# Optimization experiments

Hardware: AMD Instinct MI355X
Metric: run time of the kernel (lower is better)

Reference implementation:

```python
import jax, jax.numpy as jnp
import numpy as np

N = 50000
E = 800000
IN_DIM = 128
HEADS = 4
OUT_DIM = 32
LEAKY_ALPHA = 0.4
BN_EPS = 1e-5


def setup_inputs() -> dict:
    key = jax.random.key(0)
    k_x, k_e, k_w, k_as, k_at = jax.random.split(key, 5)
    x = jax.random.normal(k_x, (N, IN_DIM), dtype=jnp.float32)
    edge_index = jax.random.randint(k_e, (2, E), 0, N, dtype=jnp.int32)
    # Linear weight stored as (in_dim, heads*out_dim) so that h = x @ W
    w_bound = 1.0 / np.sqrt(IN_DIM)
    W = jax.random.uniform(k_w, (IN_DIM, HEADS * OUT_DIM), dtype=jnp.float32,
                           minval=-w_bound, maxval=w_bound)
    # xavier_uniform with gain=1.414 on (heads, out_dim)
    xav = 1.414 * np.sqrt(6.0 / (HEADS + OUT_DIM))
    a_src = jax.random.uniform(k_as, (HEADS, OUT_DIM), dtype=jnp.float32, minval=-xav, maxval=xav)
    a_tgt = jax.random.uniform(k_at, (HEADS, OUT_DIM), dtype=jnp.float32, minval=-xav, maxval=xav)
    # BatchNorm affine params (fresh init: gamma=1, beta=0)
    gamma = jnp.ones((HEADS * OUT_DIM,), dtype=jnp.float32)
    beta = jnp.zeros((HEADS * OUT_DIM,), dtype=jnp.float32)
    return {"x": x, "W": W, "a_src": a_src, "a_tgt": a_tgt,
            "gamma": gamma, "beta": beta, "edge_index": edge_index}


def reference(x, W, a_src, a_tgt, gamma, beta, edge_index):
    src = edge_index[0]
    tgt = edge_index[1]
    n = x.shape[0]
    # Linear projection -> (N, H, D)
    h = (x @ W).reshape(n, HEADS, OUT_DIM)
    h_src = h[src]   # (E, H, D)
    h_tgt = h[tgt]   # (E, H, D)
    # Per-edge, per-head attention logits
    e_src = jnp.einsum('ehd,hd->eh', h_src, a_src)
    e_tgt = jnp.einsum('ehd,hd->eh', h_tgt, a_tgt)
    e = jax.nn.leaky_relu(e_src + e_tgt, negative_slope=LEAKY_ALPHA)
    # Global (per-head) max subtraction for numerical stability, as in original
    e = e - jnp.max(e, axis=0, keepdims=True)
    alpha = jnp.exp(e)  # (E, H)
    # Segment softmax denominator over target nodes
    alpha_sum = jax.ops.segment_sum(alpha, tgt, num_segments=n) + 1e-16  # (N, H)
    alpha = alpha / alpha_sum[tgt]
    # dropout is identity in eval mode
    # Weighted aggregation of source features into targets
    h_prime = h_src * alpha[:, :, None]  # (E, H, D)
    out = jax.ops.segment_sum(h_prime, tgt, num_segments=n)  # (N, H, D)
    out = out.reshape(n, HEADS * OUT_DIM)  # concat=True
    # BatchNorm1d in training mode: biased batch statistics
    mean = jnp.mean(out, axis=0)
    var = jnp.mean(jnp.square(out - mean), axis=0)
    out = (out - mean) * jax.lax.rsqrt(var + BN_EPS) * gamma + beta
    return out
```

## Files before the change

### kernel.cpp

```cpp
#include <hip/hip_runtime.h>
#include <math.h>

#define N_NODES 50000
#define E_EDGES 800000
#define IN_DIM 128
#define HEADS 4
#define OUT_DIM 32
#define HD 128
#define LEAKY 0.4f
#define BN_EPS 1e-5f

#define BSH 7
#define NB ((N_NODES + 127) >> BSH)
#define FB 196
#define FCH 4096
#define PCAP 2560
#define SRTCAP 3072
#define SCCH ((NB + 63) / 64)
#define K1B ((N_NODES + 63) / 64)
#define K2_BLOCKS 32

typedef __attribute__((ext_vector_type(8))) short short8;
typedef __attribute__((ext_vector_type(8))) unsigned short us8;
typedef __attribute__((ext_vector_type(4))) float f32x4;

__device__ __forceinline__ unsigned enc_max(float f) {
    unsigned u = __float_as_uint(f);
    return ((int)u >= 0) ? (u | 0x80000000u) : ~u;
}
__device__ __forceinline__ float dec_max(unsigned u) {
    return (u & 0x80000000u) ? __uint_as_float(u ^ 0x80000000u)
                             : __uint_as_float(~u);
}

__device__ __forceinline__ float leaky(float v) {
    return v > 0.f ? v : LEAKY * v;
}

__device__ __forceinline__ unsigned short f2bf(float f) {
    unsigned u = __float_as_uint(f);
    u = (u + 0x7FFFu + ((u >> 16) & 1u)) >> 16;
    return (unsigned short)u;
}
__device__ __forceinline__ float bf2f(unsigned short u) {
    return __uint_as_float(((unsigned)u) << 16);
}

struct FillSh { int est[FCH]; int hist[NB]; int rbase[NB]; };
union F1Sh { unsigned short Wl[32 * 64 * 8]; FillSh fl; };

__global__ __launch_bounds__(256) void f1_gemm_fill(
    const float* __restrict__ x, const float* __restrict__ W,
    const float* __restrict__ a_src, const float* __restrict__ a_tgt,
    const int* __restrict__ src, const int* __restrict__ tgt,
    int* __restrict__ bcur, int* __restrict__ ebkt,
    unsigned short* __restrict__ hb, float* __restrict__ s,
    float* __restrict__ t)
{
    __shared__ F1Sh sh;
    const int tid = threadIdx.x;

    if (blockIdx.x >= K1B) {
        int* est   = sh.fl.est;
        int* hist  = sh.fl.hist;
        int* rbase = sh.fl.rbase;
        int beg = (blockIdx.x - K1B) * FCH;
        int cnt = min(beg + FCH, E_EDGES) - beg;
        for (int i = tid; i < NB; i += 256) hist[i] = 0;
        __syncthreads();
        for (int j = tid; j < cnt; j += 256) {
            int sv = src[beg + j], tv = tgt[beg + j];
            est[j] = sv | (tv << 16);
            atomicAdd(&hist[tv >> BSH], 1);
        }
        __syncthreads();
        for (int i = tid; i < NB; i += 256) {
            int c = hist[i];
            if (c) {
                int r = atomicAdd(&bcur[i], c);
                rbase[i] = i * PCAP + min(r, PCAP);
            }
        }
        __syncthreads();
        for (int i = tid; i < NB; i += 256) hist[i] = 0;
        __syncthreads();
        for (int j = tid; j < cnt; j += 256) {
            int p  = est[j];
            int tv = (int)((unsigned)p >> 16);
            int b  = tv >> BSH;
            int off = atomicAdd(&hist[b], 1);
            int idx = rbase[b] + off;
            if (idx < (b + 1) * PCAP)
                ebkt[idx] = (p & 0xFFFF) | ((tv & 127) << 16);
        }
        return;
    }

    unsigned short* Wl = sh.Wl;
    for (int idx = tid; idx < 2048; idx += 256) {
        int l  = idx & 63;
        int f  = idx >> 6;
        int nt = f >> 2, kc = f & 3;
        int kbase = kc * 32 + ((l >> 4) << 3);
        int col   = nt * 16 + (l & 15);
        unsigned short* dst = &Wl[idx * 8];
#pragma unroll
        for (int j = 0; j < 8; j++)
            dst[j] = f2bf(W[(kbase + j) * HD + col]);
    }
    __syncthreads();

    const int wave = tid >> 6, lane = tid & 63;
    const int quad = lane >> 4, rl = lane & 15;
    const int row0 = blockIdx.x * 64 + wave * 16;
    const int crow = min(row0 + rl, N_NODES - 1);

    short8 a[4];
    const float* xp = x + (size_t)crow * IN_DIM + quad * 8;
#pragma unroll
    for (int kc = 0; kc < 4; kc++) {
        float4 v0 = *(const float4*)(xp + kc * 32);
        float4 v1 = *(const float4*)(xp + kc * 32 + 4);
        short8 av;
        av[0] = (short)f2bf(v0.x); av[1] = (short)f2bf(v0.y);
        av[2] = (short)f2bf(v0.z); av[3] = (short)f2bf(v0.w);
        av[4] = (short)f2bf(v1.x); av[5] = (short)f2bf(v1.y);
        av[6] = (short)f2bf(v1.z); av[7] = (short)f2bf(v1.w);
        a[kc] = av;
    }

    float asv[8], atv[8];
#pragma unroll
    for (int nt = 0; nt < 8; nt++) {
        asv[nt] = a_src[nt * 16 + rl];
        atv[nt] = a_tgt[nt * 16 + rl];
    }

    float ps[4][4], pt[4][4];
#pragma unroll
    for (int hh = 0; hh < 4; hh++)
#pragma unroll
        for (int r = 0; r < 4; r++) { ps[hh][r] = 0.f; pt[hh][r] = 0.f; }

#pragma unroll
    for (int nt = 0; nt < 8; nt++) {
        f32x4 acc = {0.f, 0.f, 0.f, 0.f};
#pragma unroll
        for (int kc = 0; kc < 4; kc++) {
            short8 b = *(const short8*)&Wl[((nt * 4 + kc) * 64 + lane) * 8];
            acc = __builtin_amdgcn_mfma_f32_16x16x32_bf16(a[kc], b, acc, 0, 0, 0);
        }
        const int ocol = nt * 16 + rl;
        const int hh   = nt >> 1;
#pragma unroll
        for (int r = 0; r < 4; r++) {
            int orow = row0 + quad * 4 + r;
            if (orow < N_NODES)
                hb[(size_t)orow * HD + ocol] = f2bf(acc[r]);
            ps[hh][r] = fmaf(acc[r], asv[nt], ps[hh][r]);
            pt[hh][r] = fmaf(acc[r], atv[nt], pt[hh][r]);
        }
    }

#pragma unroll
    for (int m = 1; m <= 8; m <<= 1) {
#pragma unroll
        for (int hh = 0; hh < 4; hh++)
#pragma unroll
            for (int r = 0; r < 4; r++) {
                ps[hh][r] += __shfl_xor(ps[hh][r], m, 64);
                pt[hh][r] += __shfl_xor(pt[hh][r], m, 64);
            }
    }
    if (rl == 0) {
#pragma unroll
        for (int r = 0; r < 4; r++) {
            int orow = row0 + quad * 4 + r;
            if (orow < N_NODES) {
#pragma unroll
                for (int hh = 0; hh < 4; hh++) {
                    s[orow * HEADS + hh] = ps[hh][r];
                    t[orow * HEADS + hh] = pt[hh][r];
                }
            }
        }
    }
}

struct SortSh {
    int ebl[SRTCAP]; int srt[SRTCAP]; int csc[NB + 1];
    int bins[128]; int deg_l[128]; int excl_l[128]; int cur_l[128];
    int wtot; int btot;
};
union F2Sh { SortSh so; float red[4][8]; };

__global__ __launch_bounds__(256) void f2_sort_max(
    const int* __restrict__ bcur, const int* __restrict__ ebkt,
    int* __restrict__ rowptr, unsigned short* __restrict__ esrc,
    const float* __restrict__ s, const float* __restrict__ t,
    unsigned* __restrict__ smax, unsigned* __restrict__ tmax)
{
    __shared__ F2Sh sh;
    int tid  = threadIdx.x;
    int lane = tid & 63, wv = tid >> 6;

    if (blockIdx.x >= NB) {
        int bI = blockIdx.x - NB;
        float sm0 = -INFINITY, sm1 = -INFINITY, sm2 = -INFINITY, sm3 = -INFINITY;
        float tm0 = -INFINITY, tm1 = -INFINITY, tm2 = -INFINITY, tm3 = -INFINITY;
        for (int n = bI * 256 + tid; n < N_NODES; n += K2_BLOCKS * 256) {
            float4 s4 = ((const float4*)s)[n];
            float4 t4 = ((const float4*)t)[n];
            sm0 = fmaxf(sm0, s4.x); sm1 = fmaxf(sm1, s4.y);
            sm2 = fmaxf(sm2, s4.z); sm3 = fmaxf(sm3, s4.w);
            tm0 = fmaxf(tm0, t4.x); tm1 = fmaxf(tm1, t4.y);
            tm2 = fmaxf(tm2, t4.z); tm3 = fmaxf(tm3, t4.w);
        }
#pragma unroll
        for (int m = 32; m >= 1; m >>= 1) {
            sm0 = fmaxf(sm0, __shfl_xor(sm0, m, 64));
            sm1 = fmaxf(sm1, __shfl_xor(sm1, m, 64));
            sm2 = fmaxf(sm2, __shfl_xor(sm2, m, 64));
            sm3 = fmaxf(sm3, __shfl_xor(sm3, m, 64));
            tm0 = fmaxf(tm0, __shfl_xor(tm0, m, 64));
            tm1 = fmaxf(tm1, __shfl_xor(tm1, m, 64));
            tm2 = fmaxf(tm2, __shfl_xor(tm2, m, 64));
            tm3 = fmaxf(tm3, __shfl_xor(tm3, m, 64));
        }
        if (lane == 0) {
            sh.red[wv][0] = sm0; sh.red[wv][1] = sm1;
            sh.red[wv][2] = sm2; sh.red[wv][3] = sm3;
            sh.red[wv][4] = tm0; sh.red[wv][5] = tm1;
            sh.red[wv][6] = tm2; sh.red[wv][7] = tm3;
        }
        __syncthreads();
        if (tid < 8) {
            float v = fmaxf(fmaxf(sh.red[0][tid], sh.red[1][tid]),
                            fmaxf(sh.red[2][tid], sh.red[3][tid]));
            unsigned* dst = (tid < 4) ? &smax[tid] : &tmax[tid - 4];
            atomicMax(dst, enc_max(v));
        }
        return;
    }

    int b = blockIdx.x;
    int* ebl    = sh.so.ebl;
    int* srt    = sh.so.srt;
    int* csc    = sh.so.csc;
    int* bins   = sh.so.bins;
    int* deg_l  = sh.so.deg_l;
    int* excl_l = sh.so.excl_l;
    int* cur_l  = sh.so.cur_l;

    for (int i = tid; i < NB; i += 256) csc[i] = min(bcur[i], PCAP);
    if (tid < 128) { deg_l[tid] = 0; cur_l[tid] = 0; bins[tid] = 0; }
    __syncthreads();
    if (tid < 64) {
        int cb = tid * SCCH;
        int loc[SCCH];
        int sum = 0;
#pragma unroll
        for (int k = 0; k < SCCH; k++) {
            int idx = cb + k;
            int v = (idx < NB) ? csc[idx] : 0;
            loc[k] = sum; sum += v;
        }
        int ss = sum;
#pragma unroll
        for (int off = 1; off < 64; off <<= 1) {
            int u = __shfl_up(ss, off, 64);
            if (tid >= off) ss += u;
        }
        int excl = ss - sum;
#pragma unroll
        for (int k = 0; k < SCCH; k++) {
            int idx = cb + k;
            if (idx < NB) csc[idx] = excl + loc[k];
        }
        if (tid == 63) {
            csc[NB] = excl + sum;
            if (b == 0) rowptr[N_NODES] = excl + sum;
        }
    }
    __syncthreads();
    int base_in = b * PCAP;
    int base    = csc[b];
    int cnt     = csc[b + 1] - base;

    for (int j = tid; j < cnt; j += 256) {
        int p = ebkt[base_in + j];
        ebl[j] = p;
        atomicAdd(&bins[(p & 0xFFFF) >> 9], 1);
    }
    __syncthreads();
    {
        int v = (tid < 128) ? bins[tid] : 0;
        int ssv = v;
#pragma unroll
        for (int off = 1; off < 64; off <<= 1) {
            int u = __shfl_up(ssv, off, 64);
            if (lane >= off) ssv += u;
        }
        if (tid == 63) sh.so.btot = ssv;
        __syncthreads();
        if (tid < 128) bins[tid] = ssv - v + ((wv == 1) ? sh.so.btot : 0);
        __syncthreads();
    }
    for (int j = tid; j < cnt; j += 256) {
        int p = ebl[j];
        int pos = atomicAdd(&bins[(p & 0xFFFF) >> 9], 1);
        srt[pos] = p;
    }
    __syncthreads();
    for (int j = tid; j < cnt; j += 256)
        atomicAdd(&deg_l[srt[j] >> 16], 1);
    __syncthreads();

    int v = (tid < 128) ? deg_l[tid] : 0;
    int sv2 = v;
#pragma unroll
    for (int off = 1; off < 64; off <<= 1) {
        int u = __shfl_up(sv2, off, 64);
        if (lane >= off) sv2 += u;
    }
    if (tid == 63) sh.so.wtot = sv2;
    __syncthreads();
    if (tid < 128) {
        int ex = sv2 - v + ((wv == 1) ? sh.so.wtot : 0);
        excl_l[tid] = ex;
        int node = (b << BSH) + tid;
        if (node < N_NODES) rowptr[node] = base + ex;
    }
    __syncthreads();
    for (int j = tid; j < cnt; j += 256) {
        int p  = srt[j];
        int tl = p >> 16;
        int off = atomicAdd(&cur_l[tl], 1);
        esrc[base + excl_l[tl] + off] = (unsigned short)(p & 0xFFFF);
    }
}

__global__ __launch_bounds__(256) void k4_pull(
    const int* __restrict__ rowptr, const unsigned short* __restrict__ esrc,
    const float* __restrict__ s, const float* __restrict__ t,
    const unsigned* __restrict__ smax, const unsigned* __restrict__ tmax,
    const unsigned short* __restrict__ hb, unsigned short* __restrict__ outpb)
{
    int g = blockIdx.x * 256 + threadIdx.x;
    int node = g >> 4;
    int lane = g & 15;
    if (node >= N_NODES) return;
    int head = lane >> 2;
    int beg = rowptr[node];
    int end = rowptr[node + 1];
    float mx = leaky(dec_max(smax[head]) + dec_max(tmax[head]));
    float tv = t[node * HEADS + head];

    float p0 = 0.f, p1 = 0.f, p2 = 0.f, p3 = 0.f;
    float p4 = 0.f, p5 = 0.f, p6 = 0.f, p7 = 0.f, psum = 0.f;
    float q0 = 0.f, q1 = 0.f, q2 = 0.f, q3 = 0.f;
    float q4 = 0.f, q5 = 0.f, q6 = 0.f, q7 = 0.f, qsum = 0.f;
    const unsigned short* hbase = hb + lane * 8;

    for (int j = beg; j < end; j += 8) {
        int lim = end - j;
        int si[8];
#pragma unroll
        for (int u = 0; u < 8; u++) {
            int uu = (u < lim) ? u : (lim - 1);
            si[u] = esrc[j + uu];
        }
        float sv[8];
        us8 hv[8];
#pragma unroll
        for (int u = 0; u < 8; u++) {
            sv[u] = s[si[u] * HEADS + head];
            hv[u] = *(const us8*)(hbase + (size_t)si[u] * HD);
        }
        float al[8];
#pragma unroll
        for (int u = 0; u < 8; u++) {
            float a = __expf(leaky(sv[u] + tv) - mx);
            al[u] = (u < lim) ? a : 0.f;
        }
#pragma unroll
        for (int u = 0; u < 8; u += 2) {
            float a0 = al[u], a1 = al[u + 1];
            p0 = fmaf(a0, bf2f(hv[u][0]), p0);  q0 = fmaf(a1, bf2f(hv[u+1][0]), q0);
            p1 = fmaf(a0, bf2f(hv[u][1]), p1);  q1 = fmaf(a1, bf2f(hv[u+1][1]), q1);
            p2 = fmaf(a0, bf2f(hv[u][2]), p2);  q2 = fmaf(a1, bf2f(hv[u+1][2]), q2);
            p3 = fmaf(a0, bf2f(hv[u][3]), p3);  q3 = fmaf(a1, bf2f(hv[u+1][3]), q3);
            p4 = fmaf(a0, bf2f(hv[u][4]), p4);  q4 = fmaf(a1, bf2f(hv[u+1][4]), q4);
            p5 = fmaf(a0, bf2f(hv[u][5]), p5);  q5 = fmaf(a1, bf2f(hv[u+1][5]), q5);
            p6 = fmaf(a0, bf2f(hv[u][6]), p6);  q6 = fmaf(a1, bf2f(hv[u+1][6]), q6);
            p7 = fmaf(a0, bf2f(hv[u][7]), p7);  q7 = fmaf(a1, bf2f(hv[u+1][7]), q7);
            psum += a0; qsum += a1;
        }
    }

    float w = 1.0f / (psum + qsum + 1e-16f);
    us8 o;
    o[0] = f2bf((p0 + q0) * w); o[1] = f2bf((p1 + q1) * w);
    o[2] = f2bf((p2 + q2) * w); o[3] = f2bf((p3 + q3) * w);
    o[4] = f2bf((p4 + q4) * w); o[5] = f2bf((p5 + q5) * w);
    o[6] = f2bf((p6 + q6) * w); o[7] = f2bf((p7 + q7) * w);
    *(us8*)(outpb + (size_t)node * HD + lane * 8) = o;
}

__global__ __launch_bounds__(256) void k5_stats(
    const unsigned short* __restrict__ outpb,
    float* __restrict__ bnsum, float* __restrict__ bnsq)
{
    __shared__ float lsum[HD], lsq[HD];
    int c8  = threadIdx.x & 15;
    int grp = threadIdx.x >> 4;
    if (threadIdx.x < HD) { lsum[threadIdx.x] = 0.f; lsq[threadIdx.x] = 0.f; }
    __syncthreads();
    int base = blockIdx.x * 256;
    int end  = min(base + 256, N_NODES);
    float sm[8], sq[8];
#pragma unroll
    for (int i = 0; i < 8; i++) { sm[i] = 0.f; sq[i] = 0.f; }
    for (int r = base + grp; r < end; r += 16) {
        us8 v = *(const us8*)(outpb + (size_t)r * HD + c8 * 8);
#pragma unroll
        for (int i = 0; i < 8; i++) {
            float f = bf2f(v[i]);
            sm[i] += f;
            sq[i] = fmaf(f, f, sq[i]);
        }
    }
#pragma unroll
    for (int i = 0; i < 8; i++) {
        atomicAdd(&lsum[c8 * 8 + i], sm[i]);
        atomicAdd(&lsq[c8 * 8 + i], sq[i]);
    }
    __syncthreads();
    if (threadIdx.x < HD) {
        unsafeAtomicAdd(&bnsum[threadIdx.x], lsum[threadIdx.x]);
        unsafeAtomicAdd(&bnsq[threadIdx.x], lsq[threadIdx.x]);
    }
}

__global__ __launch_bounds__(256) void k6_apply(
    const unsigned short* __restrict__ outpb,
    const float* __restrict__ bnsum, const float* __restrict__ bnsq,
    const float* __restrict__ gamma, const float* __restrict__ beta,
    float* __restrict__ out)
{
    int c8  = threadIdx.x & 15;
    int grp = threadIdx.x >> 4;
    int base = blockIdx.x * 256;
    int end  = min(base + 256, N_NODES);
    float inv_n = 1.0f / (float)N_NODES;
    float scale[8], shift[8];
#pragma unroll
    for (int i = 0; i < 8; i++) {
        int c = c8 * 8 + i;
        float mean = bnsum[c] * inv_n;
        float var  = bnsq[c] * inv_n - mean * mean;
        float sc   = gamma[c] * rsqrtf(var + BN_EPS);
        scale[i] = sc;
        shift[i] = beta[c] - mean * sc;
    }
    for (int r = base + grp; r < end; r += 16) {
        us8 v = *(const us8*)(outpb + (size_t)r * HD + c8 * 8);
        float4 o0, o1;
        o0.x = fmaf(bf2f(v[0]), scale[0], shift[0]);
        o0.y = fmaf(bf2f(v[1]), scale[1], shift[1]);
        o0.z = fmaf(bf2f(v[2]), scale[2], shift[2]);
        o0.w = fmaf(bf2f(v[3]), scale[3], shift[3]);
        o1.x = fmaf(bf2f(v[4]), scale[4], shift[4]);
        o1.y = fmaf(bf2f(v[5]), scale[5], shift[5]);
        o1.z = fmaf(bf2f(v[6]), scale[6], shift[6]);
        o1.w = fmaf(bf2f(v[7]), scale[7], shift[7]);
        float* op = out + (size_t)r * HD + c8 * 8;
        ((float4*)op)[0] = o0;
        ((float4*)op)[1] = o1;
    }
}

extern "C" void kernel_launch(void* const* d_in, const int* in_sizes, int n_in,
                              void* d_out, int out_size, void* d_ws, size_t ws_size,
                              hipStream_t stream)
{
    const float* x     = (const float*)d_in[0];
    const float* W     = (const float*)d_in[1];
    const float* a_src = (const float*)d_in[2];
    const float* a_tgt = (const float*)d_in[3];
    const float* gamma = (const float*)d_in[4];
    const float* beta  = (const float*)d_in[5];
    const int*   eidx  = (const int*)d_in[6];
    const int* src = eidx;
    const int* tgt = eidx + E_EDGES;
    float* out = (float*)d_out;

    unsigned short* hb    = (unsigned short*)d_ws;
    float*          s     = (float*)d_ws + 3200000;
    float*          t     = s + (size_t)N_NODES * HEADS;
    unsigned short* outpb = (unsigned short*)(t + (size_t)N_NODES * HEADS);
    int*            ebkt  = (int*)outpb;
    unsigned short* esrc  = outpb + 6400000;
    int*            rowptr= (int*)(esrc + E_EDGES);
    int*      bcur  = rowptr + N_NODES + 1;
    unsigned* smax  = (unsigned*)(bcur + 392);
    unsigned* tmax  = smax + 4;
    float*    bnsum = (float*)(tmax + 4);
    float*    bnsq  = bnsum + HD;
    size_t zero_bytes = (392 + 8 + HD + HD) * 4;
    hipMemsetAsync(bcur, 0, zero_bytes, stream);

    f1_gemm_fill<<<K1B + FB, 256, 0, stream>>>(x, W, a_src, a_tgt,
                                               src, tgt, bcur, ebkt,
                                               hb, s, t);
    f2_sort_max<<<NB + K2_BLOCKS, 256, 0, stream>>>(bcur, ebkt, rowptr, esrc,
                                                    s, t, smax, tmax);
    long long k4_threads = (long long)N_NODES * 16;
    k4_pull<<<(unsigned)((k4_threads + 255) / 256), 256, 0, stream>>>(
        rowptr, esrc, s, t, smax, tmax, hb, outpb);
    k5_stats<<<(N_NODES + 255) / 256, 256, 0, stream>>>(outpb, bnsum, bnsq);
    k6_apply<<<(N_NODES + 255) / 256, 256, 0, stream>>>(outpb, bnsum, bnsq,
                                                        gamma, beta, out);
}
```

Before: 178.4 us.

## Split projected features into per-head slices and aggregate one head per launch

The projected feature matrix is stored head-major, as four contiguous N×32 bf16 slices. The pull aggregation becomes four launches, one per head, each touching only a 3.2 MB slice, so the gathered working set fits better in cache. The sort kernel also drops the intra-bucket source-bin counting sort and builds CSR directly from the bucketed edges. This gives up source locality within each segment and adds three kernel launches, and each edge's index list is now re-read once per head.

```diff
diff --git a/kernel.cpp b/kernel.cpp
--- a/kernel.cpp
+++ b/kernel.cpp
@@ -15,10 +15,10 @@
 #define FB 196
 #define FCH 4096
 #define PCAP 2560
-#define SRTCAP 3072
 #define SCCH ((NB + 63) / 64)
 #define K1B ((N_NODES + 63) / 64)
 #define K2_BLOCKS 32
+#define HSL (N_NODES * 32)
 
 typedef __attribute__((ext_vector_type(8))) short short8;
 typedef __attribute__((ext_vector_type(8))) unsigned short us8;
@@ -150,13 +150,13 @@
             short8 b = *(const short8*)&Wl[((nt * 4 + kc) * 64 + lane) * 8];
             acc = __builtin_amdgcn_mfma_f32_16x16x32_bf16(a[kc], b, acc, 0, 0, 0);
         }
-        const int ocol = nt * 16 + rl;
         const int hh   = nt >> 1;
+        const int colh = (nt & 1) * 16 + rl;
 #pragma unroll
         for (int r = 0; r < 4; r++) {
             int orow = row0 + quad * 4 + r;
             if (orow < N_NODES)
-                hb[(size_t)orow * HD + ocol] = f2bf(acc[r]);
+                hb[(size_t)hh * HSL + (size_t)orow * 32 + colh] = f2bf(acc[r]);
             ps[hh][r] = fmaf(acc[r], asv[nt], ps[hh][r]);
             pt[hh][r] = fmaf(acc[r], atv[nt], pt[hh][r]);
         }
@@ -188,9 +188,9 @@
 }
 
 struct SortSh {
-    int ebl[SRTCAP]; int srt[SRTCAP]; int csc[NB + 1];
-    int bins[128]; int deg_l[128]; int excl_l[128]; int cur_l[128];
-    int wtot; int btot;
+    int ebl[PCAP]; int csc[NB + 1];
+    int deg_l[128]; int excl_l[128]; int cur_l[128];
+    int wtot;
 };
 union F2Sh { SortSh so; float red[4][8]; };
 
@@ -245,15 +245,13 @@
 
     int b = blockIdx.x;
     int* ebl    = sh.so.ebl;
-    int* srt    = sh.so.srt;
     int* csc    = sh.so.csc;
-    int* bins   = sh.so.bins;
     int* deg_l  = sh.so.deg_l;
     int* excl_l = sh.so.excl_l;
     int* cur_l  = sh.so.cur_l;
 
     for (int i = tid; i < NB; i += 256) csc[i] = min(bcur[i], PCAP);
-    if (tid < 128) { deg_l[tid] = 0; cur_l[tid] = 0; bins[tid] = 0; }
+    if (tid < 128) { deg_l[tid] = 0; cur_l[tid] = 0; }
     __syncthreads();
     if (tid < 64) {
         int cb = tid * SCCH;
@@ -290,30 +288,8 @@
     for (int j = tid; j < cnt; j += 256) {
         int p = ebkt[base_in + j];
         ebl[j] = p;
-        atomicAdd(&bins[(p & 0xFFFF) >> 9], 1);
-    }
-    __syncthreads();
-    {
-        int v = (tid < 128) ? bins[tid] : 0;
-        int ssv = v;
-#pragma unroll
-        for (int off = 1; off < 64; off <<= 1) {
-            int u = __shfl_up(ssv, off, 64);
-            if (lane >= off) ssv += u;
-        }
-        if (tid == 63) sh.so.btot = ssv;
-        __syncthreads();
-        if (tid < 128) bins[tid] = ssv - v + ((wv == 1) ? sh.so.btot : 0);
-        __syncthreads();
-    }
-    for (int j = tid; j < cnt; j += 256) {
-        int p = ebl[j];
-        int pos = atomicAdd(&bins[(p & 0xFFFF) >> 9], 1);
-        srt[pos] = p;
-    }
-    __syncthreads();
-    for (int j = tid; j < cnt; j += 256)
-        atomicAdd(&deg_l[srt[j] >> 16], 1);
+        atomicAdd(&deg_l[p >> 16], 1);
+    }
     __syncthreads();
 
     int v = (tid < 128) ? deg_l[tid] : 0;
@@ -333,24 +309,24 @@
     }
     __syncthreads();
     for (int j = tid; j < cnt; j += 256) {
-        int p  = srt[j];
+        int p  = ebl[j];
         int tl = p >> 16;
         int off = atomicAdd(&cur_l[tl], 1);
         esrc[base + excl_l[tl] + off] = (unsigned short)(p & 0xFFFF);
     }
 }
 
-__global__ __launch_bounds__(256) void k4_pull(
+__global__ __launch_bounds__(256) void k4_pull_head(
     const int* __restrict__ rowptr, const unsigned short* __restrict__ esrc,
     const float* __restrict__ s, const float* __restrict__ t,
     const unsigned* __restrict__ smax, const unsigned* __restrict__ tmax,
-    const unsigned short* __restrict__ hb, unsigned short* __restrict__ outpb)
+    const unsigned short* __restrict__ hb, unsigned short* __restrict__ outpb,
+    int head)
 {
     int g = blockIdx.x * 256 + threadIdx.x;
-    int node = g >> 4;
-    int lane = g & 15;
+    int node = g >> 2;
+    int lane = g & 3;
     if (node >= N_NODES) return;
-    int head = lane >> 2;
     int beg = rowptr[node];
     int end = rowptr[node + 1];
     float mx = leaky(dec_max(smax[head]) + dec_max(tmax[head]));
@@ -360,31 +336,31 @@
     float p4 = 0.f, p5 = 0.f, p6 = 0.f, p7 = 0.f, psum = 0.f;
     float q0 = 0.f, q1 = 0.f, q2 = 0.f, q3 = 0.f;
     float q4 = 0.f, q5 = 0.f, q6 = 0.f, q7 = 0.f, qsum = 0.f;
-    const unsigned short* hbase = hb + lane * 8;
-
-    for (int j = beg; j < end; j += 8) {
+    const unsigned short* hsl = hb + (size_t)head * HSL + lane * 8;
+
+    for (int j = beg; j < end; j += 4) {
         int lim = end - j;
-        int si[8];
-#pragma unroll
-        for (int u = 0; u < 8; u++) {
+        int si[4];
+#pragma unroll
+        for (int u = 0; u < 4; u++) {
             int uu = (u < lim) ? u : (lim - 1);
             si[u] = esrc[j + uu];
         }
-        float sv[8];
-        us8 hv[8];
-#pragma unroll
-        for (int u = 0; u < 8; u++) {
+        float sv[4];
+        us8 hv[4];
+#pragma unroll
+        for (int u = 0; u < 4; u++) {
             sv[u] = s[si[u] * HEADS + head];
-            hv[u] = *(const us8*)(hbase + (size_t)si[u] * HD);
-        }
-        float al[8];
-#pragma unroll
-        for (int u = 0; u < 8; u++) {
+            hv[u] = *(const us8*)(hsl + (size_t)si[u] * 32);
+        }
+        float al[4];
+#pragma unroll
+        for (int u = 0; u < 4; u++) {
             float a = __expf(leaky(sv[u] + tv) - mx);
             al[u] = (u < lim) ? a : 0.f;
         }
 #pragma unroll
-        for (int u = 0; u < 8; u += 2) {
+        for (int u = 0; u < 4; u += 2) {
             float a0 = al[u], a1 = al[u + 1];
             p0 = fmaf(a0, bf2f(hv[u][0]), p0);  q0 = fmaf(a1, bf2f(hv[u+1][0]), q0);
             p1 = fmaf(a0, bf2f(hv[u][1]), p1);  q1 = fmaf(a1, bf2f(hv[u+1][1]), q1);
@@ -404,7 +380,7 @@
     o[2] = f2bf((p2 + q2) * w); o[3] = f2bf((p3 + q3) * w);
     o[4] = f2bf((p4 + q4) * w); o[5] = f2bf((p5 + q5) * w);
     o[6] = f2bf((p6 + q6) * w); o[7] = f2bf((p7 + q7) * w);
-    *(us8*)(outpb + (size_t)node * HD + lane * 8) = o;
+    *(us8*)(outpb + (size_t)node * HD + head * 32 + lane * 8) = o;
 }
 
 __global__ __launch_bounds__(256) void k5_stats(
@@ -515,9 +491,9 @@
                                                hb, s, t);
     f2_sort_max<<<NB + K2_BLOCKS, 256, 0, stream>>>(bcur, ebkt, rowptr, esrc,
                                                     s, t, smax, tmax);
-    long long k4_threads = (long long)N_NODES * 16;
-    k4_pull<<<(unsigned)((k4_threads + 255) / 256), 256, 0, stream>>>(
-        rowptr, esrc, s, t, smax, tmax, hb, outpb);
+    for (int h = 0; h < HEADS; ++h)
+        k4_pull_head<<<(N_NODES * 4 + 255) / 256, 256, 0, stream>>>(
+            rowptr, esrc, s, t, smax, tmax, hb, outpb, h);
     k5_stats<<<(N_NODES + 255) / 256, 256, 0, stream>>>(outpb, bnsum, bnsq);
     k6_apply<<<(N_NODES + 255) / 256, 256, 0, stream>>>(outpb, bnsum, bnsq,
                                                         gamma, beta, out);
```

After: 208.1 us. 1.17x slower.

## Local-sort edges by bucket in fill, drop per-bucket source sort, nontemporal pull I/O

Applied to the files above, without the earlier changes.

The fill kernel now does a shared-memory counting sort of each edge chunk by target bucket before writing it out, so writes to each bucket region are contiguous and need no per-edge global-offset atomics. The second kernel no longer sorts each bucket's edges by source range before grouping them by target. It counts degrees directly from the loaded list and scatters into CSR order, which removes several passes, barriers and a shared array. The pull kernel uses nontemporal loads for edge indices and nontemporal stores for its output. The cost is that edges within a target row lose their source-sorted order, which can hurt gather locality in the pull kernel, and the fill kernel uses more shared memory per block.

```diff
diff --git a/kernel.cpp b/kernel.cpp
--- a/kernel.cpp
+++ b/kernel.cpp
@@ -15,7 +15,6 @@
 #define FB 196
 #define FCH 4096
 #define PCAP 2560
-#define SRTCAP 3072
 #define SCCH ((NB + 63) / 64)
 #define K1B ((N_NODES + 63) / 64)
 #define K2_BLOCKS 32
@@ -46,7 +45,13 @@
     return __uint_as_float(((unsigned)u) << 16);
 }
 
-struct FillSh { int est[FCH]; int hist[NB]; int rbase[NB]; };
+struct FillSh {
+    int est[FCH];
+    int srt[FCH];
+    int hist[NB];
+    int lsc[NB];
+    int rbase[NB];
+};
 union F1Sh { unsigned short Wl[32 * 64 * 8]; FillSh fl; };
 
 __global__ __launch_bounds__(256) void f1_gemm_fill(
@@ -62,7 +67,9 @@
 
     if (blockIdx.x >= K1B) {
         int* est   = sh.fl.est;
+        int* srt   = sh.fl.srt;
         int* hist  = sh.fl.hist;
+        int* lsc   = sh.fl.lsc;
         int* rbase = sh.fl.rbase;
         int beg = (blockIdx.x - K1B) * FCH;
         int cnt = min(beg + FCH, E_EDGES) - beg;
@@ -81,15 +88,43 @@
                 rbase[i] = i * PCAP + min(r, PCAP);
             }
         }
+        if (tid < 64) {
+            int cb = tid * SCCH;
+            int loc[SCCH];
+            int sum = 0;
+#pragma unroll
+            for (int k = 0; k < SCCH; k++) {
+                int idx = cb + k;
+                int v = (idx < NB) ? hist[idx] : 0;
+                loc[k] = sum; sum += v;
+            }
+            int ss = sum;
+#pragma unroll
+            for (int off = 1; off < 64; off <<= 1) {
+                int u = __shfl_up(ss, off, 64);
+                if (tid >= off) ss += u;
+            }
+            int excl = ss - sum;
+#pragma unroll
+            for (int k = 0; k < SCCH; k++) {
+                int idx = cb + k;
+                if (idx < NB) lsc[idx] = excl + loc[k];
+            }
+        }
         __syncthreads();
-        for (int i = tid; i < NB; i += 256) hist[i] = 0;
+        for (int i = tid; i < NB; i += 256) hist[i] = lsc[i];
         __syncthreads();
         for (int j = tid; j < cnt; j += 256) {
-            int p  = est[j];
+            int p = est[j];
+            int pos = atomicAdd(&hist[(int)((unsigned)p >> 16) >> BSH], 1);
+            srt[pos] = p;
+        }
+        __syncthreads();
+        for (int j = tid; j < cnt; j += 256) {
+            int p  = srt[j];
             int tv = (int)((unsigned)p >> 16);
             int b  = tv >> BSH;
-            int off = atomicAdd(&hist[b], 1);
-            int idx = rbase[b] + off;
+            int idx = rbase[b] + (j - lsc[b]);
             if (idx < (b + 1) * PCAP)
                 ebkt[idx] = (p & 0xFFFF) | ((tv & 127) << 16);
         }
@@ -188,9 +223,9 @@
 }
 
 struct SortSh {
-    int ebl[SRTCAP]; int srt[SRTCAP]; int csc[NB + 1];
-    int bins[128]; int deg_l[128]; int excl_l[128]; int cur_l[128];
-    int wtot; int btot;
+    int ebl[PCAP]; int csc[NB + 1];
+    int deg_l[128]; int excl_l[128]; int cur_l[128];
+    int wtot;
 };
 union F2Sh { SortSh so; float red[4][8]; };
 
@@ -245,15 +280,13 @@
 
     int b = blockIdx.x;
     int* ebl    = sh.so.ebl;
-    int* srt    = sh.so.srt;
     int* csc    = sh.so.csc;
-    int* bins   = sh.so.bins;
     int* deg_l  = sh.so.deg_l;
     int* excl_l = sh.so.excl_l;
     int* cur_l  = sh.so.cur_l;
 
     for (int i = tid; i < NB; i += 256) csc[i] = min(bcur[i], PCAP);
-    if (tid < 128) { deg_l[tid] = 0; cur_l[tid] = 0; bins[tid] = 0; }
+    if (tid < 128) { deg_l[tid] = 0; cur_l[tid] = 0; }
     __syncthreads();
     if (tid < 64) {
         int cb = tid * SCCH;
@@ -290,30 +323,8 @@
     for (int j = tid; j < cnt; j += 256) {
         int p = ebkt[base_in + j];
         ebl[j] = p;
-        atomicAdd(&bins[(p & 0xFFFF) >> 9], 1);
-    }
-    __syncthreads();
-    {
-        int v = (tid < 128) ? bins[tid] : 0;
-        int ssv = v;
-#pragma unroll
-        for (int off = 1; off < 64; off <<= 1) {
-            int u = __shfl_up(ssv, off, 64);
-            if (lane >= off) ssv += u;
-        }
-        if (tid == 63) sh.so.btot = ssv;
-        __syncthreads();
-        if (tid < 128) bins[tid] = ssv - v + ((wv == 1) ? sh.so.btot : 0);
-        __syncthreads();
-    }
-    for (int j = tid; j < cnt; j += 256) {
-        int p = ebl[j];
-        int pos = atomicAdd(&bins[(p & 0xFFFF) >> 9], 1);
-        srt[pos] = p;
-    }
-    __syncthreads();
-    for (int j = tid; j < cnt; j += 256)
-        atomicAdd(&deg_l[srt[j] >> 16], 1);
+        atomicAdd(&deg_l[p >> 16], 1);
+    }
     __syncthreads();
 
     int v = (tid < 128) ? deg_l[tid] : 0;
@@ -333,7 +344,7 @@
     }
     __syncthreads();
     for (int j = tid; j < cnt; j += 256) {
-        int p  = srt[j];
+        int p  = ebl[j];
         int tl = p >> 16;
         int off = atomicAdd(&cur_l[tl], 1);
         esrc[base + excl_l[tl] + off] = (unsigned short)(p & 0xFFFF);
@@ -368,7 +379,7 @@
 #pragma unroll
         for (int u = 0; u < 8; u++) {
             int uu = (u < lim) ? u : (lim - 1);
-            si[u] = esrc[j + uu];
+            si[u] = __builtin_nontemporal_load(&esrc[j + uu]);
         }
         float sv[8];
         us8 hv[8];
@@ -404,7 +415,7 @@
     o[2] = f2bf((p2 + q2) * w); o[3] = f2bf((p3 + q3) * w);
     o[4] = f2bf((p4 + q4) * w); o[5] = f2bf((p5 + q5) * w);
     o[6] = f2bf((p6 + q6) * w); o[7] = f2bf((p7 + q7) * w);
-    *(us8*)(outpb + (size_t)node * HD + lane * 8) = o;
+    __builtin_nontemporal_store(o, (us8*)(outpb + (size_t)node * HD + lane * 8));
 }
 
 __global__ __launch_bounds__(256) void k5_stats(
```

After: 177.5 us, median of 2. About the same (-0.5%).
